# Performance work log

Measured on AMD Instinct MI355X. Metric: run time of the kernel, lower is better.

Reference implementation:

```python
import jax, jax.numpy as jnp
import numpy as np

N = 50000          # nodes
E = 800000         # edges
F_IN, H, OUT = 512, 256, 2
BN_EPS = 1e-5


def setup_inputs() -> dict:
    key = jax.random.key(0)
    ks = jax.random.split(key, 10)
    x = jax.random.normal(ks[0], (N, F_IN), jnp.float32)
    edge_index = jax.random.randint(ks[1], (2, E), 0, N, dtype=jnp.int64)
    edge_weight = jax.random.uniform(ks[2], (E,), jnp.float32)

    def lin(k, fan_in, fan_out):
        return jax.random.normal(k, (fan_in, fan_out), jnp.float32) / np.sqrt(fan_in).astype(np.float32)

    W1, b1 = lin(ks[3], F_IN, H), jnp.zeros((H,), jnp.float32)
    W2, b2 = lin(ks[4], H, H), jnp.zeros((H,), jnp.float32)
    W3, b3 = lin(ks[5], H, OUT), jnp.zeros((OUT,), jnp.float32)
    # BatchNorm1d affine params + running stats (eval mode)
    g1, be1 = jnp.ones((H,), jnp.float32), jnp.zeros((H,), jnp.float32)
    m1 = 0.1 * jax.random.normal(ks[6], (H,), jnp.float32)
    v1 = jax.random.uniform(ks[7], (H,), jnp.float32, 0.5, 1.5)
    g2, be2 = jnp.ones((H,), jnp.float32), jnp.zeros((H,), jnp.float32)
    m2 = 0.1 * jax.random.normal(ks[8], (H,), jnp.float32)
    v2 = jax.random.uniform(ks[9], (H,), jnp.float32, 0.5, 1.5)
    return {"x": x, "edge_index": edge_index, "edge_weight": edge_weight,
            "W1": W1, "b1": b1, "g1": g1, "be1": be1, "m1": m1, "v1": v1,
            "W2": W2, "b2": b2, "g2": g2, "be2": be2, "m2": m2, "v2": v2,
            "W3": W3, "b3": b3}


def gcn_conv(x, row, col, w, W, b):
    # PyG GCNConv (eval): h = x @ W; out[col] += norm * h[row]; + b
    # row/col/w already include self-loops with weight 1.
    n = x.shape[0]
    h = x @ W                                      # [N, out]
    deg = jax.ops.segment_sum(w, col, num_segments=n)
    dinv = jnp.where(deg > 0, jax.lax.rsqrt(deg), 0.0)
    norm = dinv[row] * w * dinv[col]               # [E+N]
    out = jax.ops.segment_sum(h[row] * norm[:, None], col, num_segments=n)
    return out + b


def batchnorm_eval(x, g, be, m, v):
    return (x - m) * jax.lax.rsqrt(v + BN_EPS) * g + be


def reference(x, edge_index, edge_weight, W1, b1, g1, be1, m1, v1,
              W2, b2, g2, be2, m2, v2, W3, b3):
    n = x.shape[0]
    loops = jnp.arange(n, dtype=edge_index.dtype)
    row = jnp.concatenate([edge_index[0], loops])
    col = jnp.concatenate([edge_index[1], loops])
    w = jnp.concatenate([edge_weight, jnp.ones((n,), x.dtype)])

    h = jax.nn.relu(batchnorm_eval(gcn_conv(x, row, col, w, W1, b1), g1, be1, m1, v1))
    h = jax.nn.relu(batchnorm_eval(gcn_conv(h, row, col, w, W2, b2), g2, be2, m2, v2))
    return gcn_conv(h, row, col, w, W3, b3)
```

## Files before the change

### kernel.cpp

```cpp
#include <hip/hip_runtime.h>
#include <stdint.h>

#define F_IN 512
#define HF 256
#define OUT_F 2
#define BN_EPS 1e-5f
#define SCAN_B 256
#define LDSTR 36

typedef __attribute__((ext_vector_type(8))) short bf16x8;
typedef __attribute__((ext_vector_type(4))) float f32x4;

__device__ inline float bf2f(unsigned short u) {
    union { float f; uint32_t i; } v; v.i = ((uint32_t)u) << 16; return v.f;
}
__device__ inline unsigned short f2bf(float f) {
    union { float f; uint32_t i; } v; v.f = f;
    uint32_t r = v.i + 0x7FFFu + ((v.i >> 16) & 1u);
    return (unsigned short)(r >> 16);
}

__global__ void prep_kernel(unsigned long long* __restrict__ packed,
                            const float* __restrict__ W1, unsigned short* __restrict__ W1t,
                            const float* __restrict__ W2, unsigned short* __restrict__ W2t,
                            unsigned short* __restrict__ xbf_pad,
                            unsigned short* __restrict__ bufa_pad,
                            int n, int padx, int pada) {
    int idx = blockIdx.x * blockDim.x + threadIdx.x;
    if (idx < n) { packed[idx] = 1ULL << 20; return; }
    int j = idx - n;
    if (j < F_IN * HF) {
        int nn = j >> 9, k = j & (F_IN - 1);
        W1t[j] = f2bf(W1[(size_t)k * HF + nn]);
        return;
    }
    j -= F_IN * HF;
    if (j < HF * HF) {
        int nn = j >> 8, k = j & (HF - 1);
        W2t[j] = f2bf(W2[(size_t)k * HF + nn]);
        return;
    }
    j -= HF * HF;
    if (j < padx) { xbf_pad[j] = 0; return; }
    j -= padx;
    if (j < pada) bufa_pad[j] = 0;
}

__global__ void count_conv_kernel(const int* __restrict__ col,
                                  const float* __restrict__ w,
                                  unsigned long long* __restrict__ packed,
                                  const float* __restrict__ x,
                                  unsigned short* __restrict__ xbf,
                                  int e, int nchunk) {
    int tid = blockIdx.x * blockDim.x + threadIdx.x;
    if (tid < e) {
        unsigned long long add = (1ULL << 40)
            | (unsigned long long)__float2uint_rn(w[tid] * 1048576.0f);
        atomicAdd(&packed[col[tid]], add);
    }
    const int stride = gridDim.x * blockDim.x;
    const float4* x4 = (const float4*)x;
    for (int c = tid; c < nchunk; c += stride) {
        float4 f0 = x4[2 * c];
        float4 f1 = x4[2 * c + 1];
        bf16x8 v;
        v[0] = (short)f2bf(f0.x); v[1] = (short)f2bf(f0.y);
        v[2] = (short)f2bf(f0.z); v[3] = (short)f2bf(f0.w);
        v[4] = (short)f2bf(f1.x); v[5] = (short)f2bf(f1.y);
        v[6] = (short)f2bf(f1.z); v[7] = (short)f2bf(f1.w);
        *(bf16x8*)(xbf + (size_t)c * 8) = v;
    }
}

__global__ __launch_bounds__(256)
void gemm_kernel(const unsigned short* __restrict__ A,
                 const unsigned short* __restrict__ Bt,
                 unsigned short* __restrict__ C, int K) {
    __shared__ unsigned short As[2][128 * LDSTR];
    __shared__ unsigned short Bs[2][128 * LDSTR];
    const int tid  = threadIdx.x;
    const int lane = tid & 63;
    const int wv   = tid >> 6;
    const int wrow = wv >> 1, wcol = wv & 1;
    const int m0 = blockIdx.x * 128;
    const int n0 = blockIdx.y * 128;

    const int sr = tid >> 2;
    const int sc = (tid & 3) * 8;

    const unsigned short* pa0 = A + (size_t)(m0 + sr) * K + sc;
    const unsigned short* pa1 = A + (size_t)(m0 + sr + 64) * K + sc;
    const unsigned short* pb0 = Bt + (size_t)(n0 + sr) * K + sc;
    const unsigned short* pb1 = Bt + (size_t)(n0 + sr + 64) * K + sc;

    f32x4 zero4 = {0.0f, 0.0f, 0.0f, 0.0f};
    f32x4 acc[4][4];
    #pragma unroll
    for (int i = 0; i < 4; ++i)
        #pragma unroll
        for (int j = 0; j < 4; ++j) acc[i][j] = zero4;

    const int q8 = (lane >> 4) * 8;
    const int ml = lane & 15;

    bf16x8 va0 = *(const bf16x8*)pa0;
    bf16x8 va1 = *(const bf16x8*)pa1;
    bf16x8 vb0 = *(const bf16x8*)pb0;
    bf16x8 vb1 = *(const bf16x8*)pb1;

    const int nsteps = K >> 5;
    for (int s = 0; s < nsteps; ++s) {
        const int buf = s & 1;
        *(bf16x8*)&As[buf][sr * LDSTR + sc]        = va0;
        *(bf16x8*)&As[buf][(sr + 64) * LDSTR + sc] = va1;
        *(bf16x8*)&Bs[buf][sr * LDSTR + sc]        = vb0;
        *(bf16x8*)&Bs[buf][(sr + 64) * LDSTR + sc] = vb1;
        __syncthreads();
        if (s + 1 < nsteps) {
            int off = (s + 1) * 32;
            va0 = *(const bf16x8*)(pa0 + off);
            va1 = *(const bf16x8*)(pa1 + off);
            vb0 = *(const bf16x8*)(pb0 + off);
            vb1 = *(const bf16x8*)(pb1 + off);
        }
        bf16x8 af[4], bfr[4];
        #pragma unroll
        for (int i = 0; i < 4; ++i)
            af[i] = *(const bf16x8*)&As[buf][(wrow * 64 + i * 16 + ml) * LDSTR + q8];
        #pragma unroll
        for (int j = 0; j < 4; ++j)
            bfr[j] = *(const bf16x8*)&Bs[buf][(wcol * 64 + j * 16 + ml) * LDSTR + q8];
        #pragma unroll
        for (int i = 0; i < 4; ++i)
            #pragma unroll
            for (int j = 0; j < 4; ++j)
                acc[i][j] = __builtin_amdgcn_mfma_f32_16x16x32_bf16(af[i], bfr[j], acc[i][j], 0, 0, 0);
    }

    const int q4 = (lane >> 4) * 4;
    #pragma unroll
    for (int i = 0; i < 4; ++i) {
        #pragma unroll
        for (int j = 0; j < 4; ++j) {
            #pragma unroll
            for (int rg = 0; rg < 4; ++rg) {
                int r = m0 + wrow * 64 + i * 16 + q4 + rg;
                int c = n0 + wcol * 64 + j * 16 + ml;
                C[(size_t)r * HF + c] = f2bf(acc[i][j][rg]);
            }
        }
    }
}

__global__ void scan1_kernel(const unsigned long long* __restrict__ packed,
                             int* __restrict__ local, int* __restrict__ blocksum, int n) {
    __shared__ int tmp[SCAN_B];
    int i = blockIdx.x * SCAN_B + threadIdx.x;
    int v = (i < n) ? (int)(packed[i] >> 40) : 0;
    tmp[threadIdx.x] = v;
    __syncthreads();
    for (int off = 1; off < SCAN_B; off <<= 1) {
        int t = 0;
        if ((int)threadIdx.x >= off) t = tmp[threadIdx.x - off];
        __syncthreads();
        if ((int)threadIdx.x >= off) tmp[threadIdx.x] += t;
        __syncthreads();
    }
    if (i < n) local[i] = tmp[threadIdx.x] - v;
    if (threadIdx.x == SCAN_B - 1) blocksum[blockIdx.x] = tmp[SCAN_B - 1];
}

__global__ void scan3_dinv_kernel(int* __restrict__ csr_ptr, int* __restrict__ cursor,
                                  const int* __restrict__ blocksum,
                                  const unsigned long long* __restrict__ packed,
                                  float* __restrict__ dinv, int n, int e, int nb) {
    __shared__ int red[SCAN_B];
    int t = threadIdx.x;
    red[t] = (t < nb && t < (int)blockIdx.x) ? blocksum[t] : 0;
    __syncthreads();
    for (int off = SCAN_B / 2; off > 0; off >>= 1) {
        if (t < off) red[t] += red[t + off];
        __syncthreads();
    }
    int prefix = red[0];
    int i = blockIdx.x * SCAN_B + t;
    if (i < n) {
        int val = csr_ptr[i] + prefix;
        csr_ptr[i] = val;
        cursor[i] = val;
        float deg = (float)(packed[i] & 0xFFFFFFFFFFULL) * (1.0f / 1048576.0f);
        dinv[i] = rsqrtf(deg);
    }
    if (i == 0) csr_ptr[n] = e;
}

__global__ void fill_kernel(const int* __restrict__ row, const int* __restrict__ col,
                            const float* __restrict__ w, const float* __restrict__ dinv,
                            int* __restrict__ cursor, int2* __restrict__ csr_edge, int e) {
    int i = blockIdx.x * blockDim.x + threadIdx.x;
    if (i < e) {
        int r = row[i], c = col[i];
        int pos = atomicAdd(&cursor[c], 1);
        float nrm = dinv[r] * w[i] * dinv[c];
        csr_edge[pos] = make_int2(r, __float_as_int(nrm));
    }
}

#define AGB 16
template<int FINAL>
__global__ void agg_kernel(const unsigned short* __restrict__ h,
                           const int* __restrict__ ptr,
                           const int2* __restrict__ edge,
                           const float* __restrict__ dinv,
                           const float* __restrict__ b, const float* __restrict__ g,
                           const float* __restrict__ be, const float* __restrict__ m,
                           const float* __restrict__ v,
                           unsigned short* __restrict__ out,
                           const float* __restrict__ W3, float* __restrict__ h3, int n) {
    int wid  = (blockIdx.x * blockDim.x + threadIdx.x) >> 6;
    int lane = threadIdx.x & 63;
    if (wid >= n) return;
    int p0 = ptr[wid], p1 = ptr[wid + 1];
    const int fo = lane * 4;
    float a0 = 0.f, a1 = 0.f, a2 = 0.f, a3 = 0.f;

    const int pend = p0 + ((p1 - p0) & ~(AGB - 1));
    for (int p = p0; p < pend; p += AGB) {
        int2 ed[AGB];
        #pragma unroll
        for (int k = 0; k < AGB; ++k) ed[k] = edge[p + k];
        ushort4 hv[AGB];
        #pragma unroll
        for (int k = 0; k < AGB; ++k)
            hv[k] = *(const ushort4*)(h + (size_t)ed[k].x * HF + fo);
        #pragma unroll
        for (int k = 0; k < AGB; ++k) {
            float nw = __int_as_float(ed[k].y);
            a0 += nw * bf2f(hv[k].x);
            a1 += nw * bf2f(hv[k].y);
            a2 += nw * bf2f(hv[k].z);
            a3 += nw * bf2f(hv[k].w);
        }
    }
    if (pend < p1) {
        int2 ed[AGB];
        float wv[AGB];
        #pragma unroll
        for (int k = 0; k < AGB; ++k) {
            int idx = pend + k < p1 ? pend + k : p1 - 1;
            ed[k] = edge[idx];
            wv[k] = (pend + k < p1) ? __int_as_float(ed[k].y) : 0.0f;
        }
        ushort4 hv[AGB];
        #pragma unroll
        for (int k = 0; k < AGB; ++k)
            hv[k] = *(const ushort4*)(h + (size_t)ed[k].x * HF + fo);
        #pragma unroll
        for (int k = 0; k < AGB; ++k) {
            a0 += wv[k] * bf2f(hv[k].x);
            a1 += wv[k] * bf2f(hv[k].y);
            a2 += wv[k] * bf2f(hv[k].z);
            a3 += wv[k] * bf2f(hv[k].w);
        }
    }
    float s = dinv[wid];
    float sl = s * s;
    ushort4 hv = *(const ushort4*)(h + (size_t)wid * HF + fo);
    a0 += sl * bf2f(hv.x);
    a1 += sl * bf2f(hv.y);
    a2 += sl * bf2f(hv.z);
    a3 += sl * bf2f(hv.w);

    float4 bb  = *(const float4*)(b + fo);
    float4 gg  = *(const float4*)(g + fo);
    float4 bee = *(const float4*)(be + fo);
    float4 mm  = *(const float4*)(m + fo);
    float4 vv  = *(const float4*)(v + fo);
    float f0 = fmaxf((a0 + bb.x - mm.x) * rsqrtf(vv.x + BN_EPS) * gg.x + bee.x, 0.f);
    float f1 = fmaxf((a1 + bb.y - mm.y) * rsqrtf(vv.y + BN_EPS) * gg.y + bee.y, 0.f);
    float f2 = fmaxf((a2 + bb.z - mm.z) * rsqrtf(vv.z + BN_EPS) * gg.z + bee.z, 0.f);
    float f3 = fmaxf((a3 + bb.w - mm.w) * rsqrtf(vv.w + BN_EPS) * gg.w + bee.w, 0.f);

    if (!FINAL) {
        ushort4 o;
        o.x = f2bf(f0); o.y = f2bf(f1); o.z = f2bf(f2); o.w = f2bf(f3);
        *(ushort4*)(out + (size_t)wid * HF + fo) = o;
    } else {
        float4 w0 = *(const float4*)(W3 + fo * 2);
        float4 w1 = *(const float4*)(W3 + fo * 2 + 4);
        float s0 = f0 * w0.x + f1 * w0.z + f2 * w1.x + f3 * w1.z;
        float s1 = f0 * w0.y + f1 * w0.w + f2 * w1.y + f3 * w1.w;
        #pragma unroll
        for (int o = 32; o > 0; o >>= 1) {
            s0 += __shfl_down(s0, o, 64);
            s1 += __shfl_down(s1, o, 64);
        }
        if (lane == 0) {
            h3[wid * 2 + 0] = s0;
            h3[wid * 2 + 1] = s1;
        }
    }
}

__global__ void out_kernel(const float* __restrict__ h3,
                           const int* __restrict__ ptr, const int2* __restrict__ edge,
                           const float* __restrict__ dinv,
                           const float* __restrict__ b3, float* __restrict__ out, int n) {
    int i = blockIdx.x * blockDim.x + threadIdx.x;
    if (i >= n) return;
    int p0 = ptr[i], p1 = ptr[i + 1];
    float a0 = 0.f, a1 = 0.f;
    for (int p = p0; p < p1; p += 4) {
        #pragma unroll
        for (int k = 0; k < 4; ++k) {
            int idx = p + k < p1 ? p + k : p1 - 1;
            int2 e = edge[idx];
            float nw = (p + k < p1) ? __int_as_float(e.y) : 0.0f;
            float2 u = *(const float2*)(h3 + 2 * e.x);
            a0 += nw * u.x;
            a1 += nw * u.y;
        }
    }
    float s = dinv[i];
    float sl = s * s;
    out[2 * i + 0] = a0 + sl * h3[2 * i + 0] + b3[0];
    out[2 * i + 1] = a1 + sl * h3[2 * i + 1] + b3[1];
}

static inline char* align16(char* p) {
    return (char*)(((uintptr_t)p + 15) & ~(uintptr_t)15);
}

extern "C" void kernel_launch(void* const* d_in, const int* in_sizes, int n_in,
                              void* d_out, int out_size, void* d_ws, size_t ws_size,
                              hipStream_t stream) {
    const float* x   = (const float*)d_in[0];
    const int*   ei  = (const int*)d_in[1];
    const float* ew  = (const float*)d_in[2];
    const float* W1  = (const float*)d_in[3];
    const float* b1  = (const float*)d_in[4];
    const float* g1  = (const float*)d_in[5];
    const float* be1 = (const float*)d_in[6];
    const float* m1  = (const float*)d_in[7];
    const float* v1  = (const float*)d_in[8];
    const float* W2  = (const float*)d_in[9];
    const float* b2  = (const float*)d_in[10];
    const float* g2  = (const float*)d_in[11];
    const float* be2 = (const float*)d_in[12];
    const float* m2  = (const float*)d_in[13];
    const float* v2  = (const float*)d_in[14];
    const float* W3  = (const float*)d_in[15];
    const float* b3  = (const float*)d_in[16];

    const int N  = in_sizes[0] / F_IN;
    const int E  = in_sizes[2];
    const int MP = (N + 127) & ~127;
    const int* row = ei;
    const int* col = ei + E;

    char* wsb = (char*)d_ws;
    unsigned long long* packed = (unsigned long long*)wsb; wsb = align16(wsb + (size_t)N * 8);
    float* dinv     = (float*)wsb;          wsb = align16(wsb + (size_t)N * 4);
    int*   csr_ptr  = (int*)wsb;            wsb = align16(wsb + (size_t)(N + 1) * 4);
    int*   cursor   = (int*)wsb;            wsb = align16(wsb + (size_t)N * 4);
    int*   blocksum = (int*)wsb;            wsb = align16(wsb + (size_t)SCAN_B * 4);
    int2*  csr_edge = (int2*)wsb;           wsb = align16(wsb + (size_t)E * 8);
    unsigned short* W1t = (unsigned short*)wsb;  wsb = align16(wsb + (size_t)F_IN * HF * 2);
    unsigned short* W2t = (unsigned short*)wsb;  wsb = align16(wsb + (size_t)HF * HF * 2);
    unsigned short* xbf  = (unsigned short*)wsb; wsb = align16(wsb + (size_t)MP * F_IN * 2);
    unsigned short* bufh = (unsigned short*)wsb; wsb = align16(wsb + (size_t)MP * HF * 2);
    unsigned short* bufa = (unsigned short*)wsb; wsb = align16(wsb + (size_t)MP * HF * 2);
    float* h3 = (float*)wsb;                wsb = align16(wsb + (size_t)N * OUT_F * 4);
    float* outf = (float*)d_out;

    const int TB = 256;
    const int nscan = (N + SCAN_B - 1) / SCAN_B;
    const int padx = (MP - N) * F_IN;
    const int pada = (MP - N) * HF;
    const int preptot = N + F_IN * HF + HF * HF + padx + pada;
    const int ncc = (E + TB - 1) / TB;
    const int nchunk = (N * F_IN) / 8;

    prep_kernel<<<(preptot + TB - 1) / TB, TB, 0, stream>>>(
        packed, W1, W1t, W2, W2t, xbf + (size_t)N * F_IN, bufa + (size_t)N * HF, N, padx, pada);

    count_conv_kernel<<<ncc, TB, 0, stream>>>(col, ew, packed, x, xbf, E, nchunk);

    scan1_kernel<<<nscan, SCAN_B, 0, stream>>>(packed, csr_ptr, blocksum, N);
    scan3_dinv_kernel<<<nscan, SCAN_B, 0, stream>>>(csr_ptr, cursor, blocksum, packed, dinv, N, E, nscan);
    fill_kernel<<<(E + TB - 1) / TB, TB, 0, stream>>>(row, col, ew, dinv, cursor, csr_edge, E);

    dim3 ggrid(MP / 128, HF / 128);

    gemm_kernel<<<ggrid, TB, 0, stream>>>(xbf, W1t, bufh, F_IN);
    agg_kernel<0><<<((size_t)N * 64 + TB - 1) / TB, TB, 0, stream>>>(
        bufh, csr_ptr, csr_edge, dinv, b1, g1, be1, m1, v1, bufa, nullptr, nullptr, N);

    gemm_kernel<<<ggrid, TB, 0, stream>>>(bufa, W2t, bufh, HF);
    agg_kernel<1><<<((size_t)N * 64 + TB - 1) / TB, TB, 0, stream>>>(
        bufh, csr_ptr, csr_edge, dinv, b2, g2, be2, m2, v2, nullptr, W3, h3, N);

    out_kernel<<<(N + TB - 1) / TB, TB, 0, stream>>>(h3, csr_ptr, csr_edge, dinv, b3, outf, N);
}
```

Before: 467.7 us.

## Split aggregation into feature slices with 8 nodes per wavefront

The aggregation kernel now gives each 8-lane group one node and one 32-feature slice. Consecutive blocks cover the 8 slices of the same 32 nodes, so the gathered neighbour rows can be reused in L2 across slices. Edge loads become nontemporal, run over the group's maximum degree with masked weights, and the tail branch is gone. The final layer writes per-slice partial W3 products that a new combine kernel sums. The costs are extra work from degree divergence inside a wavefront, each edge list being read eight times, and one more kernel launch.

```diff
diff --git a/kernel.cpp b/kernel.cpp
--- a/kernel.cpp
+++ b/kernel.cpp
@@ -7,6 +7,9 @@
 #define BN_EPS 1e-5f
 #define SCAN_B 256
 #define LDSTR 36
+#define AGB 8
+#define NSLICE 8
+#define SLICE_F 32
 
 typedef __attribute__((ext_vector_type(8))) short bf16x8;
 typedef __attribute__((ext_vector_type(4))) float f32x4;
@@ -25,6 +28,7 @@
                             const float* __restrict__ W2, unsigned short* __restrict__ W2t,
                             unsigned short* __restrict__ xbf_pad,
                             unsigned short* __restrict__ bufa_pad,
+                            int* __restrict__ epad,
                             int n, int padx, int pada) {
     int idx = blockIdx.x * blockDim.x + threadIdx.x;
     if (idx < n) { packed[idx] = 1ULL << 20; return; }
@@ -43,7 +47,9 @@
     j -= HF * HF;
     if (j < padx) { xbf_pad[j] = 0; return; }
     j -= padx;
-    if (j < pada) bufa_pad[j] = 0;
+    if (j < pada) { bufa_pad[j] = 0; return; }
+    j -= pada;
+    if (j < 2 * AGB) epad[j] = 0;
 }
 
 __global__ void count_conv_kernel(const int* __restrict__ col,
@@ -206,7 +212,6 @@
     }
 }
 
-#define AGB 16
 template<int FINAL>
 __global__ void agg_kernel(const unsigned short* __restrict__ h,
                            const int* __restrict__ ptr,
@@ -216,23 +221,40 @@
                            const float* __restrict__ be, const float* __restrict__ m,
                            const float* __restrict__ v,
                            unsigned short* __restrict__ out,
-                           const float* __restrict__ W3, float* __restrict__ h3, int n) {
-    int wid  = (blockIdx.x * blockDim.x + threadIdx.x) >> 6;
-    int lane = threadIdx.x & 63;
-    if (wid >= n) return;
-    int p0 = ptr[wid], p1 = ptr[wid + 1];
-    const int fo = lane * 4;
+                           const float* __restrict__ W3, float* __restrict__ h3p, int n) {
+    const int slice = blockIdx.x & (NSLICE - 1);
+    const int b32   = blockIdx.x >> 3;
+    const int lane  = threadIdx.x & 63;
+    const int wv    = threadIdx.x >> 6;
+    const int grp   = lane >> 3;
+    const int l     = lane & 7;
+    const int node  = b32 * 32 + wv * 8 + grp;
+    const int nodeC = node < n ? node : n - 1;
+    const int fo    = slice * SLICE_F + l * 4;
+
+    int p0  = ptr[nodeC];
+    int deg = (node < n) ? (ptr[nodeC + 1] - p0) : 0;
+    int dmax = deg;
+    dmax = max(dmax, __shfl_xor(dmax, 8, 64));
+    dmax = max(dmax, __shfl_xor(dmax, 16, 64));
+    dmax = max(dmax, __shfl_xor(dmax, 32, 64));
+
     float a0 = 0.f, a1 = 0.f, a2 = 0.f, a3 = 0.f;
 
-    const int pend = p0 + ((p1 - p0) & ~(AGB - 1));
-    for (int p = p0; p < pend; p += AGB) {
+    for (int t = 0; t < dmax; t += AGB) {
         int2 ed[AGB];
         #pragma unroll
-        for (int k = 0; k < AGB; ++k) ed[k] = edge[p + k];
+        for (int k = 0; k < AGB; ++k) {
+            int off = (t + k < deg) ? (t + k) : 0;
+            long long ev = __builtin_nontemporal_load((const long long*)(edge + p0 + off));
+            ed[k].x = (int)ev;
+            ed[k].y = (int)(ev >> 32);
+            if (t + k >= deg) ed[k].y = 0;
+        }
         ushort4 hv[AGB];
         #pragma unroll
         for (int k = 0; k < AGB; ++k)
-            hv[k] = *(const ushort4*)(h + (size_t)ed[k].x * HF + fo);
+            hv[k] = *(const ushort4*)(h + (size_t)(unsigned)ed[k].x * HF + fo);
         #pragma unroll
         for (int k = 0; k < AGB; ++k) {
             float nw = __int_as_float(ed[k].y);
@@ -242,30 +264,10 @@
             a3 += nw * bf2f(hv[k].w);
         }
     }
-    if (pend < p1) {
-        int2 ed[AGB];
-        float wv[AGB];
-        #pragma unroll
-        for (int k = 0; k < AGB; ++k) {
-            int idx = pend + k < p1 ? pend + k : p1 - 1;
-            ed[k] = edge[idx];
-            wv[k] = (pend + k < p1) ? __int_as_float(ed[k].y) : 0.0f;
-        }
-        ushort4 hv[AGB];
-        #pragma unroll
-        for (int k = 0; k < AGB; ++k)
-            hv[k] = *(const ushort4*)(h + (size_t)ed[k].x * HF + fo);
-        #pragma unroll
-        for (int k = 0; k < AGB; ++k) {
-            a0 += wv[k] * bf2f(hv[k].x);
-            a1 += wv[k] * bf2f(hv[k].y);
-            a2 += wv[k] * bf2f(hv[k].z);
-            a3 += wv[k] * bf2f(hv[k].w);
-        }
-    }
-    float s = dinv[wid];
+
+    float s = dinv[nodeC];
     float sl = s * s;
-    ushort4 hv = *(const ushort4*)(h + (size_t)wid * HF + fo);
+    ushort4 hv = *(const ushort4*)(h + (size_t)nodeC * HF + fo);
     a0 += sl * bf2f(hv.x);
     a1 += sl * bf2f(hv.y);
     a2 += sl * bf2f(hv.z);
@@ -282,24 +284,40 @@
     float f3 = fmaxf((a3 + bb.w - mm.w) * rsqrtf(vv.w + BN_EPS) * gg.w + bee.w, 0.f);
 
     if (!FINAL) {
-        ushort4 o;
-        o.x = f2bf(f0); o.y = f2bf(f1); o.z = f2bf(f2); o.w = f2bf(f3);
-        *(ushort4*)(out + (size_t)wid * HF + fo) = o;
+        unsigned long long pk =
+            (unsigned long long)f2bf(f0)
+          | ((unsigned long long)f2bf(f1) << 16)
+          | ((unsigned long long)f2bf(f2) << 32)
+          | ((unsigned long long)f2bf(f3) << 48);
+        if (node < n)
+            __builtin_nontemporal_store((long long)pk,
+                                        (long long*)(out + (size_t)node * HF + fo));
     } else {
         float4 w0 = *(const float4*)(W3 + fo * 2);
         float4 w1 = *(const float4*)(W3 + fo * 2 + 4);
         float s0 = f0 * w0.x + f1 * w0.z + f2 * w1.x + f3 * w1.z;
         float s1 = f0 * w0.y + f1 * w0.w + f2 * w1.y + f3 * w1.w;
-        #pragma unroll
-        for (int o = 32; o > 0; o >>= 1) {
-            s0 += __shfl_down(s0, o, 64);
-            s1 += __shfl_down(s1, o, 64);
-        }
-        if (lane == 0) {
-            h3[wid * 2 + 0] = s0;
-            h3[wid * 2 + 1] = s1;
-        }
-    }
+        s0 += __shfl_xor(s0, 1, 64); s1 += __shfl_xor(s1, 1, 64);
+        s0 += __shfl_xor(s0, 2, 64); s1 += __shfl_xor(s1, 2, 64);
+        s0 += __shfl_xor(s0, 4, 64); s1 += __shfl_xor(s1, 4, 64);
+        if (l == 0 && node < n) {
+            h3p[(size_t)node * 16 + slice * 2 + 0] = s0;
+            h3p[(size_t)node * 16 + slice * 2 + 1] = s1;
+        }
+    }
+}
+
+__global__ void combine_kernel(const float* __restrict__ h3p, float* __restrict__ h3, int n) {
+    int i = blockIdx.x * blockDim.x + threadIdx.x;
+    if (i >= n) return;
+    float s0 = 0.f, s1 = 0.f;
+    #pragma unroll
+    for (int s = 0; s < NSLICE; ++s) {
+        s0 += h3p[(size_t)i * 16 + s * 2 + 0];
+        s1 += h3p[(size_t)i * 16 + s * 2 + 1];
+    }
+    h3[2 * i + 0] = s0;
+    h3[2 * i + 1] = s1;
 }
 
 __global__ void out_kernel(const float* __restrict__ h3,
@@ -364,25 +382,27 @@
     int*   csr_ptr  = (int*)wsb;            wsb = align16(wsb + (size_t)(N + 1) * 4);
     int*   cursor   = (int*)wsb;            wsb = align16(wsb + (size_t)N * 4);
     int*   blocksum = (int*)wsb;            wsb = align16(wsb + (size_t)SCAN_B * 4);
-    int2*  csr_edge = (int2*)wsb;           wsb = align16(wsb + (size_t)E * 8);
+    int2*  csr_edge = (int2*)wsb;           wsb = align16(wsb + (size_t)(E + AGB) * 8);
     unsigned short* W1t = (unsigned short*)wsb;  wsb = align16(wsb + (size_t)F_IN * HF * 2);
     unsigned short* W2t = (unsigned short*)wsb;  wsb = align16(wsb + (size_t)HF * HF * 2);
     unsigned short* xbf  = (unsigned short*)wsb; wsb = align16(wsb + (size_t)MP * F_IN * 2);
     unsigned short* bufh = (unsigned short*)wsb; wsb = align16(wsb + (size_t)MP * HF * 2);
     unsigned short* bufa = (unsigned short*)wsb; wsb = align16(wsb + (size_t)MP * HF * 2);
     float* h3 = (float*)wsb;                wsb = align16(wsb + (size_t)N * OUT_F * 4);
+    float* h3p = (float*)xbf;
     float* outf = (float*)d_out;
 
     const int TB = 256;
     const int nscan = (N + SCAN_B - 1) / SCAN_B;
     const int padx = (MP - N) * F_IN;
     const int pada = (MP - N) * HF;
-    const int preptot = N + F_IN * HF + HF * HF + padx + pada;
+    const int preptot = N + F_IN * HF + HF * HF + padx + pada + 2 * AGB;
     const int ncc = (E + TB - 1) / TB;
     const int nchunk = (N * F_IN) / 8;
 
     prep_kernel<<<(preptot + TB - 1) / TB, TB, 0, stream>>>(
-        packed, W1, W1t, W2, W2t, xbf + (size_t)N * F_IN, bufa + (size_t)N * HF, N, padx, pada);
+        packed, W1, W1t, W2, W2t, xbf + (size_t)N * F_IN, bufa + (size_t)N * HF,
+        (int*)(csr_edge + E), N, padx, pada);
 
     count_conv_kernel<<<ncc, TB, 0, stream>>>(col, ew, packed, x, xbf, E, nchunk);
 
@@ -391,14 +411,17 @@
     fill_kernel<<<(E + TB - 1) / TB, TB, 0, stream>>>(row, col, ew, dinv, cursor, csr_edge, E);
 
     dim3 ggrid(MP / 128, HF / 128);
+    const int nB32 = (N + 31) / 32;
+    const int aggGrid = nB32 * NSLICE;
 
     gemm_kernel<<<ggrid, TB, 0, stream>>>(xbf, W1t, bufh, F_IN);
-    agg_kernel<0><<<((size_t)N * 64 + TB - 1) / TB, TB, 0, stream>>>(
+    agg_kernel<0><<<aggGrid, TB, 0, stream>>>(
         bufh, csr_ptr, csr_edge, dinv, b1, g1, be1, m1, v1, bufa, nullptr, nullptr, N);
 
     gemm_kernel<<<ggrid, TB, 0, stream>>>(bufa, W2t, bufh, HF);
-    agg_kernel<1><<<((size_t)N * 64 + TB - 1) / TB, TB, 0, stream>>>(
-        bufh, csr_ptr, csr_edge, dinv, b2, g2, be2, m2, v2, nullptr, W3, h3, N);
+    agg_kernel<1><<<aggGrid, TB, 0, stream>>>(
+        bufh, csr_ptr, csr_edge, dinv, b2, g2, be2, m2, v2, nullptr, W3, h3p, N);
+    combine_kernel<<<(N + TB - 1) / TB, TB, 0, stream>>>(h3p, h3, N);
 
     out_kernel<<<(N + TB - 1) / TB, TB, 0, stream>>>(h3, csr_ptr, csr_edge, dinv, b3, outf, N);
 }
```

Result: slower. 769.5 us (+64.5%).
